# Performance work log

Measured on AMD Instinct MI355X. Metric: run time of the kernel, lower is better.

The kernel has to match this reference:

```python
import jax, jax.numpy as jnp
import numpy as np


def setup_inputs() -> dict:
    key = jax.random.key(0)
    k1, k2, k3, k4 = jax.random.split(key, 4)
    B, T, C, H = 4, 4096, 1024, 64
    x = jax.random.normal(k1, (B, T, C), dtype=jnp.float32)
    Wq = jax.random.normal(k2, (C, H), dtype=jnp.float32) * (C ** -0.5)
    Wk = jax.random.normal(k3, (C, H), dtype=jnp.float32) * (C ** -0.5)
    Wv = jax.random.normal(k4, (C, H), dtype=jnp.float32) * (C ** -0.5)
    return {"x": x, "Wq": Wq, "Wk": Wk, "Wv": Wv}


def reference(x, Wq, Wk, Wv):
    B, T, C = x.shape
    q = jnp.einsum('btc,ch->bth', x, Wq)  # [B,T,H]
    k = jnp.einsum('btc,ch->bth', x, Wk)
    v = jnp.einsum('btc,ch->bth', x, Wv)
    # NOTE: original scales by C**0.5 (embed_dim), not head_size**0.5
    scale = jnp.asarray(C, x.dtype) ** 0.5
    wei = jnp.einsum('bth,bsh->bts', q, k) / scale  # [B,T,T]
    causal = jnp.tril(jnp.ones((T, T), dtype=bool))
    wei = jnp.where(causal, wei, -jnp.inf)
    wei = jax.nn.softmax(wei, axis=-1)  # dropout p=0.0 -> identity
    return jnp.einsum('bts,bsh->bth', wei, v)  # [B,T,H]
```

## Files before the change

### kernel.cpp

```cpp
#include <hip/hip_runtime.h>
#include <hip/hip_bf16.h>

typedef __bf16 bf16;
typedef __bf16 bf16x8 __attribute__((ext_vector_type(8)));
typedef __bf16 bf16x4 __attribute__((ext_vector_type(4)));
typedef float  f32x4  __attribute__((ext_vector_type(4)));

#define MFMA16(A, B, C) __builtin_amdgcn_mfma_f32_16x16x32_bf16((A), (B), (C), 0, 0, 0)

static constexpr int Bn = 4;
static constexpr int T  = 4096;
static constexpr int Cd = 1024;
static constexpr int H  = 64;
static constexpr int NG = 192;
static constexpr int CH = 8;
static constexpr int SLOTS_PER_B = 288;
static constexpr float QSCALE = 0.03125f;

__device__ inline void dma16(const void* g, void* l) {
    __builtin_amdgcn_global_load_lds(
        (const __attribute__((address_space(1))) unsigned int*)g,
        (__attribute__((address_space(3))) unsigned int*)l, 16, 0, 0);
}

__device__ inline bf16x8 cvt_bf16x8(float4 a, float4 b) {
    bf16x8 r;
    r[0] = (bf16)a.x; r[1] = (bf16)a.y; r[2] = (bf16)a.z; r[3] = (bf16)a.w;
    r[4] = (bf16)b.x; r[5] = (bf16)b.y; r[6] = (bf16)b.z; r[7] = (bf16)b.w;
    return r;
}

__global__ __launch_bounds__(256) void wt_kernel(const float* __restrict__ Wq,
                                                 const float* __restrict__ Wk,
                                                 const float* __restrict__ Wv,
                                                 bf16* __restrict__ Wt) {
    __shared__ float s[64][65];
    const int cb = blockIdx.x;
    const int m  = blockIdx.y;
    const float* W = (m == 0) ? Wq : (m == 1) ? Wk : Wv;
    for (int i = threadIdx.x; i < 64 * 64; i += 256) {
        const int c = i >> 6, h = i & 63;
        s[c][h] = W[(cb * 64 + c) * H + h];
    }
    __syncthreads();
    for (int i = threadIdx.x; i < 64 * 64; i += 256) {
        const int n = i >> 6, c = i & 63;
        Wt[(m * 64 + n) * Cd + cb * 64 + c] = (bf16)s[c][n];
    }
}

__global__ __launch_bounds__(512, 4) void proj_kernel(const float* __restrict__ x,
                                                      const bf16* __restrict__ Wt,
                                                      bf16* __restrict__ qw,
                                                      bf16* __restrict__ kw,
                                                      bf16* __restrict__ vtw) {
    const int tid  = threadIdx.x;
    const int lane = tid & 63;
    const int w    = tid >> 6;
    const int wr   = w >> 2;
    const int wc   = w & 3;
    const int ml   = lane & 15;
    const int quad = lane >> 4;

    const long r0 = (long)blockIdx.x * 32;

    __shared__ float sX[2][32][64];
    __shared__ bf16  sW[2][192][64];

    const int xrow = w * 4 + (lane >> 4);
    const float* gx = x + (r0 + xrow) * Cd + (((lane & 15) ^ (xrow & 15)) << 2);
    const int wchunk = ((lane & 7) ^ (lane >> 3)) << 3;
    const bf16* gw0 = Wt + (long)(w * 24 + 0 + (lane >> 3)) * Cd + wchunk;
    const bf16* gw1 = Wt + (long)(w * 24 + 8 + (lane >> 3)) * Cd + wchunk;
    const bf16* gw2 = Wt + (long)(w * 24 + 16 + (lane >> 3)) * Cd + wchunk;

    f32x4 acc[3];
    #pragma unroll
    for (int j = 0; j < 3; ++j) acc[j] = f32x4{0.f, 0.f, 0.f, 0.f};

    dma16(gx, &sX[0][w * 4][0]);
    dma16(gw0, &sW[0][w * 24 + 0][0]);
    dma16(gw1, &sW[0][w * 24 + 8][0]);
    dma16(gw2, &sW[0][w * 24 + 16][0]);
    __syncthreads();

    const int arow = wr * 16 + ml;
    const int brow0 = wc * 48 + ml;
    const int bsw = ml & 7;

    int buf = 0;
    for (int kb = 0; kb < Cd; kb += 64) {
        if (kb + 64 < Cd) {
            dma16(gx + kb + 64, &sX[buf ^ 1][w * 4][0]);
            dma16(gw0 + kb + 64, &sW[buf ^ 1][w * 24 + 0][0]);
            dma16(gw1 + kb + 64, &sW[buf ^ 1][w * 24 + 8][0]);
            dma16(gw2 + kb + 64, &sW[buf ^ 1][w * 24 + 16][0]);
        }

        #pragma unroll
        for (int ks = 0; ks < 2; ++ks) {
            const int ca = (ks * 8 + quad * 2) ^ ml;
            const float4 lo = *(const float4*)&sX[buf][arow][ca << 2];
            const float4 hi = *(const float4*)&sX[buf][arow][(ca ^ 1) << 2];
            const bf16x8 af = cvt_bf16x8(lo, hi);
            const int cb0 = (ks * 4 + quad) ^ bsw;
            acc[0] = MFMA16(af, *(const bf16x8*)&sW[buf][brow0 + 0][cb0 << 3], acc[0]);
            acc[1] = MFMA16(af, *(const bf16x8*)&sW[buf][brow0 + 16][cb0 << 3], acc[1]);
            acc[2] = MFMA16(af, *(const bf16x8*)&sW[buf][brow0 + 32][cb0 << 3], acc[2]);
        }

        __syncthreads();
        buf ^= 1;
    }

    const int b = (int)(r0 >> 12);
    const long rowb = r0 + wr * 16 + quad * 4;
    const int  tloc = (int)(rowb & 4095);

    #pragma unroll
    for (int f = 0; f < 3; ++f) {
        const int base = wc * 48 + f * 16;
        const int sel  = base >> 6;
        const int h    = (base & 63) + ml;
        if (sel == 0) {
            #pragma unroll
            for (int rr = 0; rr < 4; ++rr)
                qw[(rowb + rr) * H + h] = (bf16)(acc[f][rr] * QSCALE);
        } else if (sel == 1) {
            #pragma unroll
            for (int rr = 0; rr < 4; ++rr)
                kw[(rowb + rr) * H + h] = (bf16)acc[f][rr];
        } else {
            bf16x4 pv;
            #pragma unroll
            for (int rr = 0; rr < 4; ++rr) pv[rr] = (bf16)acc[f][rr];
            *(bf16x4*)(vtw + ((long)(b * H + h)) * T + tloc) = pv;
        }
    }
}

__global__ __launch_bounds__(256, 3) void attn_kernel(const bf16* __restrict__ qw,
                                                      const bf16* __restrict__ kw,
                                                      const bf16* __restrict__ vtw,
                                                      float* __restrict__ pO,
                                                      float* __restrict__ pL) {
    const int qt = blockIdx.x;
    const int c  = blockIdx.y;
    const int b  = blockIdx.z;
    const int g  = qt >> 3, r = qt & 7;
    if (c > g) return;

    const int tid  = threadIdx.x;
    const int lane = tid & 63;
    const int w    = tid >> 6;
    const int ml   = lane & 15;
    const int quad = lane >> 4;
    const int mx   = ml & 7;

    __shared__ bf16 sK[2][64][64];
    __shared__ bf16 sVt[2][64][64];
    __shared__ bf16 sP[4][16][72];

    const int t0 = qt * 64;

    const bf16* q0 = qw + ((long)b * T + t0 + w * 16 + ml) * H;
    const bf16x8 aq0 = *(const bf16x8*)(q0 + quad * 8);
    const bf16x8 aq1 = *(const bf16x8*)(q0 + 32 + quad * 8);

    f32x4 O[4];
    #pragma unroll
    for (int ht = 0; ht < 4; ++ht) O[ht] = f32x4{0.f, 0.f, 0.f, 0.f};
    float lrow[4] = {0.f, 0.f, 0.f, 0.f};

    const int trow = t0 + w * 16 + quad * 4;
    const int jt0 = c * CH;
    const int jt1 = (c == g) ? qt + 1 : (c + 1) * CH;

    const int drow = w * 8 + (lane >> 3);
    const int dsw  = ((lane & 7) ^ (drow & 7)) << 3;
    const bf16* kbase = kw + (long)b * T * H;
    const bf16* vbase = vtw + (long)b * H * T;
    const long koffA = (long)drow * H + dsw;
    const long koffB = koffA + 32 * H;
    const long voffA = (long)drow * T + dsw;
    const long voffB = voffA + (long)32 * T;

    {
        const long ks0 = (long)jt0 * 64;
        dma16(kbase + ks0 * H + koffA, &sK[0][w * 8][0]);
        dma16(kbase + ks0 * H + koffB, &sK[0][32 + w * 8][0]);
        dma16(vbase + ks0 + voffA, &sVt[0][w * 8][0]);
        dma16(vbase + ks0 + voffB, &sVt[0][32 + w * 8][0]);
    }
    __syncthreads();

    int buf = 0;
    for (int jt = jt0; jt < jt1; ++jt) {
        if (jt + 1 < jt1) {
            const long ksn = (long)(jt + 1) * 64;
            dma16(kbase + ksn * H + koffA, &sK[buf ^ 1][w * 8][0]);
            dma16(kbase + ksn * H + koffB, &sK[buf ^ 1][32 + w * 8][0]);
            dma16(vbase + ksn + voffA, &sVt[buf ^ 1][w * 8][0]);
            dma16(vbase + ksn + voffB, &sVt[buf ^ 1][32 + w * 8][0]);
        }

        const int s0 = jt * 64;
        const bool diag = (jt == qt);
        #pragma unroll
        for (int nt = 0; nt < 4; ++nt) {
            f32x4 sacc = f32x4{0.f, 0.f, 0.f, 0.f};
            sacc = MFMA16(aq0, *(const bf16x8*)&sK[buf][nt * 16 + ml][(quad ^ mx) << 3], sacc);
            sacc = MFMA16(aq1, *(const bf16x8*)&sK[buf][nt * 16 + ml][((4 + quad) ^ mx) << 3], sacc);
            const int col = s0 + nt * 16 + ml;
            #pragma unroll
            for (int rr = 0; rr < 4; ++rr) {
                const float p = (diag && col > trow + rr) ? 0.f : __expf(sacc[rr]);
                lrow[rr] += p;
                sP[w][quad * 4 + rr][nt * 16 + ml] = (bf16)p;
            }
        }
        asm volatile("s_waitcnt lgkmcnt(0)" ::: "memory");

        #pragma unroll
        for (int ks = 0; ks < 2; ++ks) {
            const bf16x8 ap = *(const bf16x8*)&sP[w][ml][ks * 32 + quad * 8];
            #pragma unroll
            for (int ht = 0; ht < 4; ++ht)
                O[ht] = MFMA16(ap,
                    *(const bf16x8*)&sVt[buf][ht * 16 + ml][(((ks << 2) + quad) ^ mx) << 3],
                    O[ht]);
        }

        __syncthreads();
        buf ^= 1;
    }

    #pragma unroll
    for (int d = 1; d < 16; d <<= 1)
        #pragma unroll
        for (int rr = 0; rr < 4; ++rr)
            lrow[rr] += __shfl_xor(lrow[rr], d, 64);

    const long slot = (long)b * SLOTS_PER_B + (long)(g + 1) * (4 * g + r) + c;
    float* po = pO + slot * 4096 + (w * 16) * 64;
    #pragma unroll
    for (int ht = 0; ht < 4; ++ht)
        #pragma unroll
        for (int rr = 0; rr < 4; ++rr)
            po[(quad * 4 + rr) * 64 + ht * 16 + ml] = O[ht][rr];
    if (ml == 0) {
        #pragma unroll
        for (int rr = 0; rr < 4; ++rr)
            pL[slot * 64 + w * 16 + quad * 4 + rr] = lrow[rr];
    }
}

__global__ __launch_bounds__(256) void combine_kernel(const float* __restrict__ pO,
                                                      const float* __restrict__ pL,
                                                      float* __restrict__ out) {
    const int qt = blockIdx.x;
    const int b  = blockIdx.y;
    const int g  = qt >> 3, r = qt & 7;
    const int nch = g + 1;
    const long slot0 = (long)b * SLOTS_PER_B + (long)(g + 1) * (4 * g + r);

    const int tid = threadIdx.x;
    const int row = tid >> 2;
    const int q4  = tid & 3;

    f32x4 o[4];
    #pragma unroll
    for (int j = 0; j < 4; ++j) o[j] = f32x4{0.f, 0.f, 0.f, 0.f};
    float l = 0.f;

    for (int cc = 0; cc < nch; ++cc) {
        const float* po = pO + (slot0 + cc) * 4096 + row * 64 + q4 * 16;
        #pragma unroll
        for (int j = 0; j < 4; ++j) o[j] += *(const f32x4*)(po + j * 4);
        l += pL[(slot0 + cc) * 64 + row];
    }
    const float inv = 1.f / l;
    float* op = out + ((long)b * T + qt * 64 + row) * H + q4 * 16;
    #pragma unroll
    for (int j = 0; j < 4; ++j) {
        f32x4 v = o[j];
        v[0] *= inv; v[1] *= inv; v[2] *= inv; v[3] *= inv;
        *(f32x4*)(op + j * 4) = v;
    }
}

extern "C" void kernel_launch(void* const* d_in, const int* in_sizes, int n_in,
                              void* d_out, int out_size, void* d_ws, size_t ws_size,
                              hipStream_t stream) {
    const float* x  = (const float*)d_in[0];
    const float* Wq = (const float*)d_in[1];
    const float* Wk = (const float*)d_in[2];
    const float* Wv = (const float*)d_in[3];
    float* out = (float*)d_out;

    char* ws = (char*)d_ws;
    const size_t WT_BYTES = (size_t)NG * Cd * sizeof(bf16);
    const size_t QK_BYTES = (size_t)Bn * T * H * sizeof(bf16);
    const size_t PO_OFF   = WT_BYTES + 3 * QK_BYTES;
    const size_t PO_BYTES = (size_t)Bn * SLOTS_PER_B * 4096 * sizeof(float);
    bf16*  Wt  = (bf16*)ws;
    bf16*  qw  = (bf16*)(ws + WT_BYTES);
    bf16*  kw  = (bf16*)(ws + WT_BYTES + QK_BYTES);
    bf16*  vtw = (bf16*)(ws + WT_BYTES + 2 * QK_BYTES);
    float* pO  = (float*)(ws + PO_OFF);
    float* pL  = (float*)(ws + PO_OFF + PO_BYTES);

    wt_kernel<<<dim3(16, 3), dim3(256), 0, stream>>>(Wq, Wk, Wv, Wt);
    proj_kernel<<<dim3((Bn * T) / 32), dim3(512), 0, stream>>>(x, Wt, qw, kw, vtw);
    attn_kernel<<<dim3(T / 64, CH, Bn), dim3(256), 0, stream>>>(qw, kw, vtw, pO, pL);
    combine_kernel<<<dim3(T / 64, Bn), dim3(256), 0, stream>>>(pO, pL, out);
}
```

Before: 153.1 us.

## Pipeline DMA waits, compact causal grid, swizzle P tile, use exp2

```diff
diff --git a/kernel.cpp b/kernel.cpp
--- a/kernel.cpp
+++ b/kernel.cpp
@@ -15,7 +15,7 @@
 static constexpr int NG = 192;
 static constexpr int CH = 8;
 static constexpr int SLOTS_PER_B = 288;
-static constexpr float QSCALE = 0.03125f;
+static constexpr float QSCALE = 0.045084220f;
 
 __device__ inline void dma16(const void* g, void* l) {
     __builtin_amdgcn_global_load_lds(
@@ -82,7 +82,6 @@
     dma16(gw0, &sW[0][w * 24 + 0][0]);
     dma16(gw1, &sW[0][w * 24 + 8][0]);
     dma16(gw2, &sW[0][w * 24 + 16][0]);
-    __syncthreads();
 
     const int arow = wr * 16 + ml;
     const int brow0 = wc * 48 + ml;
@@ -90,12 +89,19 @@
 
     int buf = 0;
     for (int kb = 0; kb < Cd; kb += 64) {
-        if (kb + 64 < Cd) {
+        const bool pre = (kb + 64 < Cd);
+        if (pre) {
             dma16(gx + kb + 64, &sX[buf ^ 1][w * 4][0]);
             dma16(gw0 + kb + 64, &sW[buf ^ 1][w * 24 + 0][0]);
             dma16(gw1 + kb + 64, &sW[buf ^ 1][w * 24 + 8][0]);
             dma16(gw2 + kb + 64, &sW[buf ^ 1][w * 24 + 16][0]);
-        }
+            asm volatile("s_waitcnt vmcnt(4)" ::: "memory");
+        } else {
+            asm volatile("s_waitcnt vmcnt(0)" ::: "memory");
+        }
+        __builtin_amdgcn_sched_barrier(0);
+        __builtin_amdgcn_s_barrier();
+        __builtin_amdgcn_sched_barrier(0);
 
         #pragma unroll
         for (int ks = 0; ks < 2; ++ks) {
@@ -109,7 +115,10 @@
             acc[2] = MFMA16(af, *(const bf16x8*)&sW[buf][brow0 + 32][cb0 << 3], acc[2]);
         }
 
-        __syncthreads();
+        if (pre) {
+            __builtin_amdgcn_sched_barrier(0);
+            __builtin_amdgcn_s_barrier();
+        }
         buf ^= 1;
     }
 
@@ -139,16 +148,19 @@
     }
 }
 
-__global__ __launch_bounds__(256, 3) void attn_kernel(const bf16* __restrict__ qw,
+__global__ __launch_bounds__(256, 4) void attn_kernel(const bf16* __restrict__ qw,
                                                       const bf16* __restrict__ kw,
                                                       const bf16* __restrict__ vtw,
                                                       float* __restrict__ pO,
                                                       float* __restrict__ pL) {
-    const int qt = blockIdx.x;
-    const int c  = blockIdx.y;
+    const int u = blockIdx.x;
+    int g = 0;
+    #pragma unroll
+    for (int gg = 1; gg < 8; ++gg) if (u >= (gg * (gg + 1)) / 2) g = gg;
+    const int c  = u - (g * (g + 1)) / 2;
+    const int r  = blockIdx.y;
     const int b  = blockIdx.z;
-    const int g  = qt >> 3, r = qt & 7;
-    if (c > g) return;
+    const int qt = g * 8 + r;
 
     const int tid  = threadIdx.x;
     const int lane = tid & 63;
@@ -159,7 +171,7 @@
 
     __shared__ bf16 sK[2][64][64];
     __shared__ bf16 sVt[2][64][64];
-    __shared__ bf16 sP[4][16][72];
+    __shared__ bf16 sP[4][16][64];
 
     const int t0 = qt * 64;
 
@@ -192,17 +204,23 @@
         dma16(vbase + ks0 + voffA, &sVt[0][w * 8][0]);
         dma16(vbase + ks0 + voffB, &sVt[0][32 + w * 8][0]);
     }
-    __syncthreads();
 
     int buf = 0;
     for (int jt = jt0; jt < jt1; ++jt) {
-        if (jt + 1 < jt1) {
+        const bool pre = (jt + 1 < jt1);
+        if (pre) {
             const long ksn = (long)(jt + 1) * 64;
             dma16(kbase + ksn * H + koffA, &sK[buf ^ 1][w * 8][0]);
             dma16(kbase + ksn * H + koffB, &sK[buf ^ 1][32 + w * 8][0]);
             dma16(vbase + ksn + voffA, &sVt[buf ^ 1][w * 8][0]);
             dma16(vbase + ksn + voffB, &sVt[buf ^ 1][32 + w * 8][0]);
-        }
+            asm volatile("s_waitcnt vmcnt(4)" ::: "memory");
+        } else {
+            asm volatile("s_waitcnt vmcnt(0)" ::: "memory");
+        }
+        __builtin_amdgcn_sched_barrier(0);
+        __builtin_amdgcn_s_barrier();
+        __builtin_amdgcn_sched_barrier(0);
 
         const int s0 = jt * 64;
         const bool diag = (jt == qt);
@@ -214,16 +232,20 @@
             const int col = s0 + nt * 16 + ml;
             #pragma unroll
             for (int rr = 0; rr < 4; ++rr) {
-                const float p = (diag && col > trow + rr) ? 0.f : __expf(sacc[rr]);
+                const float p = (diag && col > trow + rr) ? 0.f : exp2f(sacc[rr]);
                 lrow[rr] += p;
-                sP[w][quad * 4 + rr][nt * 16 + ml] = (bf16)p;
+                const int row = quad * 4 + rr;
+                const int sw  = (row & 7) ^ ((row & 8) >> 2);
+                sP[w][row][(((nt * 2 + (ml >> 3)) ^ sw) << 3) | (ml & 7)] = (bf16)p;
             }
         }
         asm volatile("s_waitcnt lgkmcnt(0)" ::: "memory");
+        __builtin_amdgcn_sched_barrier(0);
 
         #pragma unroll
         for (int ks = 0; ks < 2; ++ks) {
-            const bf16x8 ap = *(const bf16x8*)&sP[w][ml][ks * 32 + quad * 8];
+            const int pch = ((ks * 4 + quad) ^ (ml & 7) ^ ((ml & 8) >> 2)) << 3;
+            const bf16x8 ap = *(const bf16x8*)&sP[w][ml][pch];
             #pragma unroll
             for (int ht = 0; ht < 4; ++ht)
                 O[ht] = MFMA16(ap,
@@ -231,7 +253,10 @@
                     O[ht]);
         }
 
-        __syncthreads();
+        if (pre) {
+            __builtin_amdgcn_sched_barrier(0);
+            __builtin_amdgcn_s_barrier();
+        }
         buf ^= 1;
     }
 
@@ -312,6 +337,6 @@
 
     wt_kernel<<<dim3(16, 3), dim3(256), 0, stream>>>(Wq, Wk, Wv, Wt);
     proj_kernel<<<dim3((Bn * T) / 32), dim3(512), 0, stream>>>(x, Wt, qw, kw, vtw);
-    attn_kernel<<<dim3(T / 64, CH, Bn), dim3(256), 0, stream>>>(qw, kw, vtw, pO, pL);
+    attn_kernel<<<dim3(36, CH, Bn), dim3(256), 0, stream>>>(qw, kw, vtw, pO, pL);
     combine_kernel<<<dim3(T / 64, Bn), dim3(256), 0, stream>>>(pO, pL, out);
 }
```

After: 152.3 us. About the same (-0.6%).
